# Performance work log

Measured on AMD Instinct MI355X. Metric: run time of the kernel, lower is better.

## Reference

```python
import jax, jax.numpy as jnp
import numpy as np

N, E, F_IN, G = 100000, 1600000, 128, 64
H1, H2, H3 = 64, 32, 16


def _xavier(key, fan_in, fan_out):
    lim = np.sqrt(6.0 / (fan_in + fan_out))
    return jax.random.uniform(key, (fan_in, fan_out), jnp.float32, -lim, lim)


def setup_inputs() -> dict:
    key = jax.random.key(0)
    ks = jax.random.split(key, 16)
    x = jax.random.normal(ks[0], (N, F_IN), jnp.float32)
    edge_index = jax.random.randint(ks[1], (2, E), 0, N, dtype=jnp.int32)
    batch = jnp.sort(jax.random.randint(ks[2], (N,), 0, G, dtype=jnp.int32))
    d = {
        "x": x,
        "W1": _xavier(ks[3], F_IN, H1), "b1": jnp.zeros((H1,), jnp.float32),
        "W2": _xavier(ks[4], H1, H2), "b2": jnp.zeros((H2,), jnp.float32),
        "W3": _xavier(ks[5], H2, H3), "b3": jnp.zeros((H3,), jnp.float32),
        "g1": jnp.ones((H1,), jnp.float32), "be1": jnp.zeros((H1,), jnp.float32),
        "g2": jnp.ones((H2,), jnp.float32), "be2": jnp.zeros((H2,), jnp.float32),
        "g3": jnp.ones((H3,), jnp.float32), "be3": jnp.zeros((H3,), jnp.float32),
        "attn_w": _xavier(ks[6], 3 * H3, 3), "attn_b": jnp.zeros((3,), jnp.float32),
        "fc1_w": _xavier(ks[7], H3, H3), "fc1_b": jnp.zeros((H3,), jnp.float32),
        "fc2_w": _xavier(ks[8], H3, H3 // 2), "fc2_b": jnp.zeros((H3 // 2,), jnp.float32),
        "out_w": _xavier(ks[9], H3 // 2, 1), "out_b": jnp.zeros((1,), jnp.float32),
        "edge_index": edge_index,
        "batch": batch,
        "num_graphs": G,
    }
    return d


def _lrelu(z):
    return jnp.where(z > 0, z, 0.1 * z)


def _bn(h, gamma, beta, eps=1e-5):
    # BatchNorm1d forward with batch statistics (biased variance), as torch training-mode math
    m = jnp.mean(h, axis=0)
    v = jnp.mean(jnp.square(h - m), axis=0)
    return (h - m) * jax.lax.rsqrt(v + eps) * gamma + beta


def reference(x, W1, b1, W2, b2, W3, b3, g1, be1, g2, be2, g3, be3,
              attn_w, attn_b, fc1_w, fc1_b, fc2_w, fc2_b, out_w, out_b,
              edge_index, batch, num_graphs):
    src, dst = edge_index[0], edge_index[1]
    n = x.shape[0]
    # GCN degree with self-loops: deg[i] = 1 + #incoming edges
    deg = jax.ops.segment_sum(jnp.ones((src.shape[0],), x.dtype), dst, num_segments=n) + 1.0
    dis = jax.lax.rsqrt(deg)                      # deg^-1/2, [N]
    enorm = dis[src] * dis[dst]                   # per-edge norm, [E]
    selfw = dis * dis                             # self-loop norm, [N]

    def gcn(h, W, b):
        hw = h @ W                                # [N, H]
        agg = jax.ops.segment_sum(hw[src] * enorm[:, None], dst, num_segments=n)
        return agg + selfw[:, None] * hw + b

    x1 = _lrelu(_bn(gcn(x, W1, b1), g1, be1))     # dropout = identity (eval)
    x2 = _lrelu(_bn(gcn(x1, W2, b2), g2, be2))    # residual skipped: 64 != 32
    x3 = _lrelu(_bn(gcn(x2, W3, b3), g3, be3))    # residual skipped: 32 != 16

    # multi-pool over graphs
    ones_n = jnp.ones((n,), x.dtype)
    counts = jax.ops.segment_sum(ones_n, batch, num_segments=num_graphs)  # [G]
    x_sum = jax.ops.segment_sum(x3, batch, num_segments=num_graphs)       # [G, H3]
    x_mean = x_sum / jnp.maximum(counts, 1.0)[:, None]
    x_max = jax.ops.segment_max(x3, batch, num_segments=num_graphs)

    pooled = jnp.concatenate([x_mean, x_max, x_sum], axis=1)              # [G, 3*H3]
    aw = jax.nn.softmax(pooled @ attn_w + attn_b, axis=1)                 # [G, 3]
    xg = aw[:, 0:1] * x_mean + aw[:, 1:2] * x_max + aw[:, 2:3] * x_sum    # [G, H3]

    xg = _lrelu(xg @ fc1_w + fc1_b)
    xg = _lrelu(xg @ fc2_w + fc2_b)
    out = jax.nn.sigmoid(xg @ out_w + out_b)                              # [G, 1]
    return out
```

## Files before the change

kernel.cpp:

```cpp
#include <hip/hip_runtime.h>

#define GG 64
typedef unsigned long long ull;
typedef unsigned short u16;

__device__ __forceinline__ u16 f2b(float x) {
    unsigned u = __float_as_uint(x);
    return (u16)((u + 0x7FFFu + ((u >> 16) & 1u)) >> 16);
}

__device__ __forceinline__ void add8(const uint4 q, float* acc) {
    acc[0] += __uint_as_float(q.x << 16);
    acc[1] += __uint_as_float(q.x & 0xFFFF0000u);
    acc[2] += __uint_as_float(q.y << 16);
    acc[3] += __uint_as_float(q.y & 0xFFFF0000u);
    acc[4] += __uint_as_float(q.z << 16);
    acc[5] += __uint_as_float(q.z & 0xFFFF0000u);
    acc[6] += __uint_as_float(q.w << 16);
    acc[7] += __uint_as_float(q.w & 0xFFFF0000u);
}

__global__ __launch_bounds__(256) void k_hist(const int* __restrict__ dst,
                                              int* __restrict__ cnt, int E, int n) {
    const int part = blockIdx.x & 7;
    const int nblk = gridDim.x >> 3;
    const int bser = blockIdx.x >> 3;
    const int lo = (int)(((long long)part * n) >> 3);
    const int hi = (part == 7) ? n : (int)(((long long)(part + 1) * n) >> 3);
    for (int e = bser * 256 + threadIdx.x; e < E; e += nblk * 256) {
        int d = dst[e];
        if (d >= lo && d < hi) atomicAdd(&cnt[d], 1);
    }
}

__global__ void k_scanA(const int* __restrict__ cnt, int* __restrict__ rp,
                        int* __restrict__ bsum, float* __restrict__ dis, int n) {
    __shared__ int s[256];
    int i = blockIdx.x * 256 + threadIdx.x;
    int v = (i < n) ? cnt[i] : 0;
    if (i < n) dis[i] = rsqrtf((float)v + 1.0f);
    s[threadIdx.x] = v;
    __syncthreads();
    for (int off = 1; off < 256; off <<= 1) {
        int t = (threadIdx.x >= off) ? s[threadIdx.x - off] : 0;
        __syncthreads();
        s[threadIdx.x] += t;
        __syncthreads();
    }
    if (i < n) rp[i] = s[threadIdx.x] - v;
    if (threadIdx.x == 255) bsum[blockIdx.x] = s[255];
}

__global__ void k_scanB(int* __restrict__ bsum, int nb) {
    __shared__ int s[512];
    int v = (threadIdx.x < nb) ? bsum[threadIdx.x] : 0;
    s[threadIdx.x] = v;
    __syncthreads();
    for (int off = 1; off < 512; off <<= 1) {
        int t = (threadIdx.x >= off) ? s[threadIdx.x - off] : 0;
        __syncthreads();
        s[threadIdx.x] += t;
        __syncthreads();
    }
    if (threadIdx.x < nb) bsum[threadIdx.x] = s[threadIdx.x] - v;
}

__global__ void k_scanC(int* __restrict__ rp, const int* __restrict__ bsum,
                        int* __restrict__ cursor, int n, int E) {
    int i = blockIdx.x * 256 + threadIdx.x;
    if (i < n) {
        int r = rp[i] + bsum[blockIdx.x];
        rp[i] = r;
        cursor[i] = r;
    }
    if (i == 0) rp[n] = E;
}

__global__ __launch_bounds__(256) void k_scatter(const int* __restrict__ src,
                                                 const int* __restrict__ dst,
                                                 int* __restrict__ cursor,
                                                 int* __restrict__ epack, int E, int n) {
    const int part = blockIdx.x & 7;
    const int nblk = gridDim.x >> 3;
    const int bser = blockIdx.x >> 3;
    const int lo = (int)(((long long)part * n) >> 3);
    const int hi = (part == 7) ? n : (int)(((long long)(part + 1) * n) >> 3);
    for (int e = bser * 256 + threadIdx.x; e < E; e += nblk * 256) {
        int d = dst[e];
        if (d >= lo && d < hi) {
            int s = src[e];
            int pos = atomicAdd(&cursor[d], 1);
            epack[pos] = s;
        }
    }
}

template <int FIN, int FOUT, bool BN>
__global__ __launch_bounds__(256) void k_mm(const float* __restrict__ h,
                                            const float* __restrict__ W,
                                            const float* __restrict__ dis,
                                            const float* __restrict__ stats,
                                            const float* __restrict__ gma,
                                            const float* __restrict__ bta,
                                            u16* __restrict__ hw, int n) {
    constexpr int FX  = FOUT / 4;
    constexpr int TY  = 256 / FX;
    constexpr int NT  = TY * 4;
    constexpr int LDA = FIN + ((FOUT == 64) ? 2 : 1);
    __shared__ float sA[NT * LDA];
    __shared__ float sW[FIN * FOUT];
    __shared__ float sSc[FIN], sSh[FIN];

    if (BN && threadIdx.x < FIN) {
        int f = threadIdx.x;
        float inv_n = 1.0f / (float)n;
        float m = stats[f] * inv_n;
        float var = fmaxf(stats[64 + f] * inv_n - m * m, 0.f);
        float sc = rsqrtf(var + 1e-5f) * gma[f];
        sSc[f] = sc;
        sSh[f] = bta[f] - m * sc;
    }
    for (int i = threadIdx.x; i < FIN * FOUT / 4; i += 256)
        ((float4*)sW)[i] = ((const float4*)W)[i];
    if (BN) __syncthreads();

    const int node0 = blockIdx.x * NT;
    constexpr int LD4 = NT * FIN / 4 / 256;
    #pragma unroll
    for (int i = 0; i < LD4; ++i) {
        int idx4 = i * 256 + threadIdx.x;
        int row = idx4 / (FIN / 4);
        int c4  = idx4 % (FIN / 4);
        int gn  = node0 + row;
        float4 v = make_float4(0.f, 0.f, 0.f, 0.f);
        if (gn < n) v = ((const float4*)(h + (long long)gn * FIN))[c4];
        if (BN) {
            int f = c4 * 4;
            float t;
            t = fmaf(v.x, sSc[f + 0], sSh[f + 0]); v.x = t > 0.f ? t : 0.1f * t;
            t = fmaf(v.y, sSc[f + 1], sSh[f + 1]); v.y = t > 0.f ? t : 0.1f * t;
            t = fmaf(v.z, sSc[f + 2], sSh[f + 2]); v.z = t > 0.f ? t : 0.1f * t;
            t = fmaf(v.w, sSc[f + 3], sSh[f + 3]); v.w = t > 0.f ? t : 0.1f * t;
        }
        float* p = &sA[row * LDA + c4 * 4];
        p[0] = v.x; p[1] = v.y; p[2] = v.z; p[3] = v.w;
    }
    __syncthreads();

    const int tx = threadIdx.x % FX;
    const int ty = threadIdx.x / FX;
    float acc[4][4];
    #pragma unroll
    for (int i = 0; i < 4; ++i)
        #pragma unroll
        for (int j = 0; j < 4; ++j) acc[i][j] = 0.f;

    #pragma unroll 8
    for (int k = 0; k < FIN; ++k) {
        float4 wv = *((const float4*)&sW[k * FOUT + tx * 4]);
        float a0 = sA[(ty * 4 + 0) * LDA + k];
        float a1 = sA[(ty * 4 + 1) * LDA + k];
        float a2 = sA[(ty * 4 + 2) * LDA + k];
        float a3 = sA[(ty * 4 + 3) * LDA + k];
        acc[0][0] = fmaf(a0, wv.x, acc[0][0]); acc[0][1] = fmaf(a0, wv.y, acc[0][1]);
        acc[0][2] = fmaf(a0, wv.z, acc[0][2]); acc[0][3] = fmaf(a0, wv.w, acc[0][3]);
        acc[1][0] = fmaf(a1, wv.x, acc[1][0]); acc[1][1] = fmaf(a1, wv.y, acc[1][1]);
        acc[1][2] = fmaf(a1, wv.z, acc[1][2]); acc[1][3] = fmaf(a1, wv.w, acc[1][3]);
        acc[2][0] = fmaf(a2, wv.x, acc[2][0]); acc[2][1] = fmaf(a2, wv.y, acc[2][1]);
        acc[2][2] = fmaf(a2, wv.z, acc[2][2]); acc[2][3] = fmaf(a2, wv.w, acc[2][3]);
        acc[3][0] = fmaf(a3, wv.x, acc[3][0]); acc[3][1] = fmaf(a3, wv.y, acc[3][1]);
        acc[3][2] = fmaf(a3, wv.z, acc[3][2]); acc[3][3] = fmaf(a3, wv.w, acc[3][3]);
    }

    #pragma unroll
    for (int i = 0; i < 4; ++i) {
        int gn = node0 + ty * 4 + i;
        if (gn < n) {
            float dv = dis[gn];
            ushort4 o;
            o.x = f2b(acc[i][0] * dv); o.y = f2b(acc[i][1] * dv);
            o.z = f2b(acc[i][2] * dv); o.w = f2b(acc[i][3] * dv);
            ((ushort4*)(hw + (long long)gn * FOUT))[tx] = o;
        }
    }
}

template <int FOUT>
__global__ __launch_bounds__(256) void k_agg(const u16* __restrict__ hwb,
                                             const int* __restrict__ epack,
                                             const int* __restrict__ rp,
                                             const float* __restrict__ dis,
                                             const float* __restrict__ bias,
                                             float* __restrict__ y,
                                             float* __restrict__ stats, int n) {
    constexpr int LPN = FOUT / 8;
    constexpr int NPB = 256 / LPN;
    constexpr int RS  = FOUT / 8;
    __shared__ float ssum[FOUT], ssq[FOUT];
    for (int i = threadIdx.x; i < FOUT; i += 256) { ssum[i] = 0.f; ssq[i] = 0.f; }
    __syncthreads();
    const int local = threadIdx.x / LPN;
    const int fq = threadIdx.x % LPN;
    const uint4* hw4 = (const uint4*)hwb;
    float b8[8];
    #pragma unroll
    for (int i = 0; i < 8; ++i) b8[i] = bias[fq * 8 + i];
    float lsum[8] = {0,0,0,0,0,0,0,0}, lsq[8] = {0,0,0,0,0,0,0,0};

    for (long long base = (long long)blockIdx.x * NPB; base < n;
         base += (long long)gridDim.x * NPB) {
        int node = (int)base + local;
        if (node >= n) continue;
        int j0 = rp[node], j1 = rp[node + 1];
        float acc[8] = {0,0,0,0,0,0,0,0};
        int j = j0;
        for (; j + 8 <= j1; j += 8) {
            int s0 = epack[j + 0], s1 = epack[j + 1];
            int s2 = epack[j + 2], s3 = epack[j + 3];
            int s4 = epack[j + 4], s5 = epack[j + 5];
            int s6 = epack[j + 6], s7 = epack[j + 7];
            uint4 q0 = hw4[(long long)s0 * RS + fq];
            uint4 q1 = hw4[(long long)s1 * RS + fq];
            uint4 q2 = hw4[(long long)s2 * RS + fq];
            uint4 q3 = hw4[(long long)s3 * RS + fq];
            uint4 q4 = hw4[(long long)s4 * RS + fq];
            uint4 q5 = hw4[(long long)s5 * RS + fq];
            uint4 q6 = hw4[(long long)s6 * RS + fq];
            uint4 q7 = hw4[(long long)s7 * RS + fq];
            add8(q0, acc); add8(q1, acc); add8(q2, acc); add8(q3, acc);
            add8(q4, acc); add8(q5, acc); add8(q6, acc); add8(q7, acc);
        }
        for (; j + 2 <= j1; j += 2) {
            int s0 = epack[j + 0], s1 = epack[j + 1];
            uint4 q0 = hw4[(long long)s0 * RS + fq];
            uint4 q1 = hw4[(long long)s1 * RS + fq];
            add8(q0, acc); add8(q1, acc);
        }
        for (; j < j1; ++j) {
            uint4 q = hw4[(long long)epack[j] * RS + fq];
            add8(q, acc);
        }
        uint4 qs = hw4[(long long)node * RS + fq];
        add8(qs, acc);
        float dv = dis[node];
        #pragma unroll
        for (int i = 0; i < 8; ++i) acc[i] = fmaf(dv, acc[i], b8[i]);
        float4* y4 = (float4*)y;
        long long o = (long long)node * (FOUT / 4) + fq * 2;
        y4[o]     = make_float4(acc[0], acc[1], acc[2], acc[3]);
        y4[o + 1] = make_float4(acc[4], acc[5], acc[6], acc[7]);
        #pragma unroll
        for (int i = 0; i < 8; ++i) {
            lsum[i] += acc[i];
            lsq[i] = fmaf(acc[i], acc[i], lsq[i]);
        }
    }
    #pragma unroll
    for (int i = 0; i < 8; ++i) {
        atomicAdd(&ssum[fq * 8 + i], lsum[i]);
        atomicAdd(&ssq[fq * 8 + i], lsq[i]);
    }
    __syncthreads();
    for (int i = threadIdx.x; i < FOUT; i += 256) {
        atomicAdd(&stats[i], ssum[i]);
        atomicAdd(&stats[64 + i], ssq[i]);
    }
}

__global__ void k_pool_graph(const float* __restrict__ yraw, const int* __restrict__ batch,
                             const float* __restrict__ stats, const float* __restrict__ gma,
                             const float* __restrict__ bta, int n,
                             float* __restrict__ psum, float* __restrict__ pmax,
                             float* __restrict__ pcnt) {
    const int g = blockIdx.x;
    const int f = threadIdx.x & 15;
    float inv_n = 1.0f / (float)n;
    float m = stats[f] * inv_n;
    float var = fmaxf(stats[64 + f] * inv_n - m * m, 0.f);
    float sc = rsqrtf(var + 1e-5f) * gma[f];
    float sh = bta[f] - m * sc;

    __shared__ int s_lo, s_hi;
    if (threadIdx.x == 0) {
        int lo = 0, hi = n;
        while (lo < hi) { int mid = (lo + hi) >> 1; if (batch[mid] < g) lo = mid + 1; else hi = mid; }
        s_lo = lo;
        hi = n;
        while (lo < hi) { int mid = (lo + hi) >> 1; if (batch[mid] < g + 1) lo = mid + 1; else hi = mid; }
        s_hi = lo;
    }
    __syncthreads();
    const int start = s_lo, end = s_hi;
    float lsum = 0.f, lmax = -3.0e38f;
    for (long long idx = (long long)start * 16 + threadIdx.x; idx < (long long)end * 16; idx += blockDim.x) {
        float t = fmaf(yraw[idx], sc, sh);
        float v = t > 0.f ? t : 0.1f * t;
        lsum += v;
        lmax = fmaxf(lmax, v);
    }
    __shared__ float ss[256], sm[256];
    ss[threadIdx.x] = lsum; sm[threadIdx.x] = lmax;
    __syncthreads();
    for (int off = 128; off >= 16; off >>= 1) {
        if (threadIdx.x < off) {
            ss[threadIdx.x] += ss[threadIdx.x + off];
            sm[threadIdx.x] = fmaxf(sm[threadIdx.x], sm[threadIdx.x + off]);
        }
        __syncthreads();
    }
    if (threadIdx.x < 16) {
        psum[g * 16 + threadIdx.x] = ss[threadIdx.x];
        pmax[g * 16 + threadIdx.x] = sm[threadIdx.x];
    }
    if (threadIdx.x == 0) pcnt[g] = (float)(end - start);
}

__global__ void k_head(const float* __restrict__ psum, const float* __restrict__ pmax,
                       const float* __restrict__ pcnt,
                       const float* __restrict__ attn_w, const float* __restrict__ attn_b,
                       const float* __restrict__ fc1_w, const float* __restrict__ fc1_b,
                       const float* __restrict__ fc2_w, const float* __restrict__ fc2_b,
                       const float* __restrict__ out_w, const float* __restrict__ out_b,
                       float* __restrict__ out) {
    int g = threadIdx.x;
    if (g >= GG) return;
    float xs[16], xm[16], xx[16];
    float c = fmaxf(pcnt[g], 1.0f);
    for (int f = 0; f < 16; ++f) {
        xs[f] = psum[(g << 4) + f];
        xm[f] = xs[f] / c;
        xx[f] = pmax[(g << 4) + f];
    }
    float lg[3];
    for (int cI = 0; cI < 3; ++cI) {
        float a = attn_b[cI];
        for (int f = 0; f < 16; ++f) {
            a += xm[f] * attn_w[f * 3 + cI];
            a += xx[f] * attn_w[(16 + f) * 3 + cI];
            a += xs[f] * attn_w[(32 + f) * 3 + cI];
        }
        lg[cI] = a;
    }
    float mx = fmaxf(lg[0], fmaxf(lg[1], lg[2]));
    float e0 = expf(lg[0] - mx), e1 = expf(lg[1] - mx), e2 = expf(lg[2] - mx);
    float inv = 1.0f / (e0 + e1 + e2);
    float a0 = e0 * inv, a1 = e1 * inv, a2 = e2 * inv;
    float xg[16];
    for (int f = 0; f < 16; ++f) xg[f] = a0 * xm[f] + a1 * xx[f] + a2 * xs[f];
    float t1[16];
    for (int j = 0; j < 16; ++j) {
        float a = fc1_b[j];
        for (int k = 0; k < 16; ++k) a += xg[k] * fc1_w[k * 16 + j];
        t1[j] = a > 0.f ? a : 0.1f * a;
    }
    float t2[8];
    for (int j = 0; j < 8; ++j) {
        float a = fc2_b[j];
        for (int k = 0; k < 16; ++k) a += t1[k] * fc2_w[k * 8 + j];
        t2[j] = a > 0.f ? a : 0.1f * a;
    }
    float o = out_b[0];
    for (int k = 0; k < 8; ++k) o += t2[k] * out_w[k];
    o = 1.0f / (1.0f + expf(-o));
    out[g] = o;
}

extern "C" void kernel_launch(void* const* d_in, const int* in_sizes, int n_in,
                              void* d_out, int out_size, void* d_ws, size_t ws_size,
                              hipStream_t stream) {
    const float* x      = (const float*)d_in[0];
    const float* W1     = (const float*)d_in[1];  const float* b1   = (const float*)d_in[2];
    const float* W2     = (const float*)d_in[3];  const float* b2   = (const float*)d_in[4];
    const float* W3     = (const float*)d_in[5];  const float* b3   = (const float*)d_in[6];
    const float* g1     = (const float*)d_in[7];  const float* be1  = (const float*)d_in[8];
    const float* g2     = (const float*)d_in[9];  const float* be2  = (const float*)d_in[10];
    const float* g3     = (const float*)d_in[11]; const float* be3  = (const float*)d_in[12];
    const float* attn_w = (const float*)d_in[13]; const float* attn_b = (const float*)d_in[14];
    const float* fc1_w  = (const float*)d_in[15]; const float* fc1_b  = (const float*)d_in[16];
    const float* fc2_w  = (const float*)d_in[17]; const float* fc2_b  = (const float*)d_in[18];
    const float* out_w  = (const float*)d_in[19]; const float* out_b  = (const float*)d_in[20];
    const int* edge_index = (const int*)d_in[21];
    const int* batch      = (const int*)d_in[22];

    const int N = in_sizes[0] / 128;
    const int E = in_sizes[21] / 2;
    const int* srcp = edge_index;
    const int* dstp = edge_index + E;
    const int nb = (N + 255) / 256;

    char* ws = (char*)d_ws;
    float* dis    = (float*)(ws);
    int*   cnt    = (int*)(ws + 0x80000);
    int*   rp     = (int*)(ws + 0x100000);
    int*   bsum   = (int*)(ws + 0x180000);
    float* stats1 = (float*)(ws + 0x182000);
    float* stats2 = stats1 + 128;
    float* stats3 = stats2 + 128;
    float* psum   = stats3 + 128;
    float* pmax   = psum + GG * 16;
    float* pcnt   = pmax + GG * 16;
    int*   epack  = (int*)(ws + 0x190000);
    float* buf1   = (float*)(ws + 0x190000 + (size_t)E * 4);
    u16*   hwb    = (u16*)(buf1 + (size_t)N * 64);

    hipMemsetAsync(cnt, 0, (size_t)N * 4, stream);
    k_hist<<<2048, 256, 0, stream>>>(dstp, cnt, E, N);
    k_scanA<<<nb, 256, 0, stream>>>(cnt, rp, bsum, dis, N);
    k_scanB<<<1, 512, 0, stream>>>(bsum, nb);
    k_scanC<<<nb, 256, 0, stream>>>(rp, bsum, cnt, N, E);
    k_scatter<<<2048, 256, 0, stream>>>(srcp, dstp, cnt, epack, E, N);
    hipMemsetAsync(stats1, 0, 3 * 512, stream);

    k_mm<128, 64, false><<<(N + 63) / 64, 256, 0, stream>>>(
        x, W1, dis, nullptr, nullptr, nullptr, hwb, N);
    k_agg<64><<<2048, 256, 0, stream>>>(hwb, epack, rp, dis, b1, buf1, stats1, N);

    k_mm<64, 32, true><<<(N + 127) / 128, 256, 0, stream>>>(
        buf1, W2, dis, stats1, g1, be1, hwb, N);
    k_agg<32><<<2048, 256, 0, stream>>>(hwb, epack, rp, dis, b2, buf1, stats2, N);

    k_mm<32, 16, true><<<(N + 255) / 256, 256, 0, stream>>>(
        buf1, W3, dis, stats2, g2, be2, hwb, N);
    k_agg<16><<<2048, 256, 0, stream>>>(hwb, epack, rp, dis, b3, buf1, stats3, N);

    k_pool_graph<<<GG, 256, 0, stream>>>(buf1, batch, stats3, g3, be3, N, psum, pmax, pcnt);
    k_head<<<1, 64, 0, stream>>>(psum, pmax, pcnt, attn_w, attn_b,
                                 fc1_w, fc1_b, fc2_w, fc2_b, out_w, out_b,
                                 (float*)d_out);
}
```

Before: 599.3 us.

## Split layer-1 aggregation into two feature-half passes and simplify histogram kernel

The 64-wide first-layer aggregation now runs as two launches, each gathering one 32-feature half of the bf16 rows. Each pass touches a smaller slice of the gathered table, which should fit better in cache for random gathers, at the cost of reading the CSR indices twice. The degree histogram also drops its 8-way destination partitioning in favour of one thread per edge with plain global atomics. That may increase atomic contention and cache-locality misses.

```diff
diff --git a/kernel.cpp b/kernel.cpp
--- a/kernel.cpp
+++ b/kernel.cpp
@@ -20,17 +20,9 @@
     acc[7] += __uint_as_float(q.w & 0xFFFF0000u);
 }
 
-__global__ __launch_bounds__(256) void k_hist(const int* __restrict__ dst,
-                                              int* __restrict__ cnt, int E, int n) {
-    const int part = blockIdx.x & 7;
-    const int nblk = gridDim.x >> 3;
-    const int bser = blockIdx.x >> 3;
-    const int lo = (int)(((long long)part * n) >> 3);
-    const int hi = (part == 7) ? n : (int)(((long long)(part + 1) * n) >> 3);
-    for (int e = bser * 256 + threadIdx.x; e < E; e += nblk * 256) {
-        int d = dst[e];
-        if (d >= lo && d < hi) atomicAdd(&cnt[d], 1);
-    }
+__global__ void k_hist(const int* __restrict__ dst, int* __restrict__ cnt, int E) {
+    int e = blockIdx.x * blockDim.x + threadIdx.x;
+    if (e < E) atomicAdd(&cnt[dst[e]], 1);
 }
 
 __global__ void k_scanA(const int* __restrict__ cnt, int* __restrict__ rp,
@@ -185,7 +177,7 @@
     }
 }
 
-template <int FOUT>
+template <int FPASS, int RS, int QOFF, int FBASE>
 __global__ __launch_bounds__(256) void k_agg(const u16* __restrict__ hwb,
                                              const int* __restrict__ epack,
                                              const int* __restrict__ rp,
@@ -193,18 +185,17 @@
                                              const float* __restrict__ bias,
                                              float* __restrict__ y,
                                              float* __restrict__ stats, int n) {
-    constexpr int LPN = FOUT / 8;
+    constexpr int LPN = FPASS / 8;
     constexpr int NPB = 256 / LPN;
-    constexpr int RS  = FOUT / 8;
-    __shared__ float ssum[FOUT], ssq[FOUT];
-    for (int i = threadIdx.x; i < FOUT; i += 256) { ssum[i] = 0.f; ssq[i] = 0.f; }
+    __shared__ float ssum[FPASS], ssq[FPASS];
+    for (int i = threadIdx.x; i < FPASS; i += 256) { ssum[i] = 0.f; ssq[i] = 0.f; }
     __syncthreads();
     const int local = threadIdx.x / LPN;
     const int fq = threadIdx.x % LPN;
     const uint4* hw4 = (const uint4*)hwb;
     float b8[8];
     #pragma unroll
-    for (int i = 0; i < 8; ++i) b8[i] = bias[fq * 8 + i];
+    for (int i = 0; i < 8; ++i) b8[i] = bias[FBASE + fq * 8 + i];
     float lsum[8] = {0,0,0,0,0,0,0,0}, lsq[8] = {0,0,0,0,0,0,0,0};
 
     for (long long base = (long long)blockIdx.x * NPB; base < n;
@@ -219,34 +210,34 @@
             int s2 = epack[j + 2], s3 = epack[j + 3];
             int s4 = epack[j + 4], s5 = epack[j + 5];
             int s6 = epack[j + 6], s7 = epack[j + 7];
-            uint4 q0 = hw4[(long long)s0 * RS + fq];
-            uint4 q1 = hw4[(long long)s1 * RS + fq];
-            uint4 q2 = hw4[(long long)s2 * RS + fq];
-            uint4 q3 = hw4[(long long)s3 * RS + fq];
-            uint4 q4 = hw4[(long long)s4 * RS + fq];
-            uint4 q5 = hw4[(long long)s5 * RS + fq];
-            uint4 q6 = hw4[(long long)s6 * RS + fq];
-            uint4 q7 = hw4[(long long)s7 * RS + fq];
+            uint4 q0 = hw4[(long long)s0 * RS + QOFF + fq];
+            uint4 q1 = hw4[(long long)s1 * RS + QOFF + fq];
+            uint4 q2 = hw4[(long long)s2 * RS + QOFF + fq];
+            uint4 q3 = hw4[(long long)s3 * RS + QOFF + fq];
+            uint4 q4 = hw4[(long long)s4 * RS + QOFF + fq];
+            uint4 q5 = hw4[(long long)s5 * RS + QOFF + fq];
+            uint4 q6 = hw4[(long long)s6 * RS + QOFF + fq];
+            uint4 q7 = hw4[(long long)s7 * RS + QOFF + fq];
             add8(q0, acc); add8(q1, acc); add8(q2, acc); add8(q3, acc);
             add8(q4, acc); add8(q5, acc); add8(q6, acc); add8(q7, acc);
         }
         for (; j + 2 <= j1; j += 2) {
             int s0 = epack[j + 0], s1 = epack[j + 1];
-            uint4 q0 = hw4[(long long)s0 * RS + fq];
-            uint4 q1 = hw4[(long long)s1 * RS + fq];
+            uint4 q0 = hw4[(long long)s0 * RS + QOFF + fq];
+            uint4 q1 = hw4[(long long)s1 * RS + QOFF + fq];
             add8(q0, acc); add8(q1, acc);
         }
         for (; j < j1; ++j) {
-            uint4 q = hw4[(long long)epack[j] * RS + fq];
+            uint4 q = hw4[(long long)epack[j] * RS + QOFF + fq];
             add8(q, acc);
         }
-        uint4 qs = hw4[(long long)node * RS + fq];
+        uint4 qs = hw4[(long long)node * RS + QOFF + fq];
         add8(qs, acc);
         float dv = dis[node];
         #pragma unroll
         for (int i = 0; i < 8; ++i) acc[i] = fmaf(dv, acc[i], b8[i]);
         float4* y4 = (float4*)y;
-        long long o = (long long)node * (FOUT / 4) + fq * 2;
+        long long o = (long long)node * (RS * 2) + (QOFF + fq) * 2;
         y4[o]     = make_float4(acc[0], acc[1], acc[2], acc[3]);
         y4[o + 1] = make_float4(acc[4], acc[5], acc[6], acc[7]);
         #pragma unroll
@@ -261,9 +252,9 @@
         atomicAdd(&ssq[fq * 8 + i], lsq[i]);
     }
     __syncthreads();
-    for (int i = threadIdx.x; i < FOUT; i += 256) {
-        atomicAdd(&stats[i], ssum[i]);
-        atomicAdd(&stats[64 + i], ssq[i]);
+    for (int i = threadIdx.x; i < FPASS; i += 256) {
+        atomicAdd(&stats[FBASE + i], ssum[i]);
+        atomicAdd(&stats[64 + FBASE + i], ssq[i]);
     }
 }
 
@@ -404,7 +395,7 @@
     u16*   hwb    = (u16*)(buf1 + (size_t)N * 64);
 
     hipMemsetAsync(cnt, 0, (size_t)N * 4, stream);
-    k_hist<<<2048, 256, 0, stream>>>(dstp, cnt, E, N);
+    k_hist<<<(E + 255) / 256, 256, 0, stream>>>(dstp, cnt, E);
     k_scanA<<<nb, 256, 0, stream>>>(cnt, rp, bsum, dis, N);
     k_scanB<<<1, 512, 0, stream>>>(bsum, nb);
     k_scanC<<<nb, 256, 0, stream>>>(rp, bsum, cnt, N, E);
@@ -413,15 +404,16 @@
 
     k_mm<128, 64, false><<<(N + 63) / 64, 256, 0, stream>>>(
         x, W1, dis, nullptr, nullptr, nullptr, hwb, N);
-    k_agg<64><<<2048, 256, 0, stream>>>(hwb, epack, rp, dis, b1, buf1, stats1, N);
+    k_agg<32, 8, 0, 0><<<2048, 256, 0, stream>>>(hwb, epack, rp, dis, b1, buf1, stats1, N);
+    k_agg<32, 8, 4, 32><<<2048, 256, 0, stream>>>(hwb, epack, rp, dis, b1, buf1, stats1, N);
 
     k_mm<64, 32, true><<<(N + 127) / 128, 256, 0, stream>>>(
         buf1, W2, dis, stats1, g1, be1, hwb, N);
-    k_agg<32><<<2048, 256, 0, stream>>>(hwb, epack, rp, dis, b2, buf1, stats2, N);
+    k_agg<32, 4, 0, 0><<<2048, 256, 0, stream>>>(hwb, epack, rp, dis, b2, buf1, stats2, N);
 
     k_mm<32, 16, true><<<(N + 255) / 256, 256, 0, stream>>>(
         buf1, W3, dis, stats2, g2, be2, hwb, N);
-    k_agg<16><<<2048, 256, 0, stream>>>(hwb, epack, rp, dis, b3, buf1, stats3, N);
+    k_agg<16, 2, 0, 0><<<2048, 256, 0, stream>>>(hwb, epack, rp, dis, b3, buf1, stats3, N);
 
     k_pool_graph<<<GG, 256, 0, stream>>>(buf1, batch, stats3, g3, be3, N, psum, pmax, pcnt);
     k_head<<<1, 64, 0, stream>>>(psum, pmax, pcnt, attn_w, attn_b,
```

New measurement: 630.4 us. +5.2%, slower.
